# Kernel tuning notes

Hardware: AMD Instinct MI355X
Metric: run time of the kernel (lower is better)

Reference implementation:

```python
import jax, jax.numpy as jnp
import numpy as np

FUTURE_K = 32
NEG_INF = -1e9  # finite large-negative to keep softmax NaN-free on fully-masked rows


def setup_inputs() -> dict:
    key = jax.random.key(0)
    hidden_states = jax.random.normal(key, (4, 2048, 1024), dtype=jnp.float32)
    return {"hidden_states": hidden_states}


def reference(hidden_states) -> jnp.ndarray:
    # Faithful vectorized version of FutureEncoder(summary_method='attention').
    # For each t: window = h[:, t+1 : min(t+1+K, S)], scores = h_t @ window^T,
    # summary_t = softmax(scores) @ window. t = S-1 (empty window) stays zero.
    B, S, D = hidden_states.shape
    offs = jnp.arange(1, FUTURE_K + 1)                 # [K]
    idx = jnp.arange(S)[:, None] + offs[None, :]       # [S, K] future indices t+1..t+K
    valid = idx < S                                     # [S, K]
    idx_c = jnp.minimum(idx, S - 1)
    fw = hidden_states[:, idx_c, :]                     # [B, S, K, D] gathered windows
    scores = jnp.einsum('bsd,bskd->bsk', hidden_states, fw)
    scores = jnp.where(valid[None, :, :], scores, NEG_INF)
    w = jax.nn.softmax(scores, axis=-1)                 # [B, S, K]
    w = jnp.where(valid[None, :, :], w, 0.0)
    out = jnp.einsum('bsk,bskd->bsd', w, fw)            # [B, S, D]
    any_valid = valid.any(axis=-1)                      # [S]; False only at t = S-1
    return jnp.where(any_valid[None, :, None], out, 0.0)
```

## Files before the change

kernel.cpp:

```cpp
#include <hip/hip_runtime.h>
#include <math.h>


constexpr int S_CONST = 2048;
constexpr int D = 1024;
constexpr int G = 16;
constexpr int NTOK = 8192;
constexpr int JW = 48;
constexpr int JP = 49;
constexpr int NW = 8;

typedef short bf16x8 __attribute__((ext_vector_type(8)));
typedef float f32x4  __attribute__((ext_vector_type(4)));
typedef unsigned int u32x4 __attribute__((ext_vector_type(4)));

__device__ inline void cvt8(float4 x0, float4 x1, bf16x8& hi, bf16x8& lo) {
    float xs[8] = {x0.x, x0.y, x0.z, x0.w, x1.x, x1.y, x1.z, x1.w};
    u32x4 hv, lv;
    #pragma unroll
    for (int p = 0; p < 4; ++p) {
        float a = xs[2 * p], b = xs[2 * p + 1];
        unsigned hp;
        asm("v_cvt_pk_bf16_f32 %0, %1, %2" : "=v"(hp) : "v"(a), "v"(b));
        float ha = __builtin_bit_cast(float, hp << 16);
        float hb = __builtin_bit_cast(float, hp & 0xffff0000u);
        float la = a - ha, lb = b - hb;
        unsigned lp;
        asm("v_cvt_pk_bf16_f32 %0, %1, %2" : "=v"(lp) : "v"(la), "v"(lb));
        hv[p] = hp; lv[p] = lp;
    }
    hi = __builtin_bit_cast(bf16x8, hv);
    lo = __builtin_bit_cast(bf16x8, lv);
}

__global__ __launch_bounds__(512, 4)
void future_encoder_kernel(const float* __restrict__ h,
                           float* __restrict__ out) {
    __shared__ float sc[NW * G * JP];
    __shared__ float wm[G * JP];

    int bid = blockIdx.x, nblk = gridDim.x, lb = bid;
    if ((nblk & 7) == 0) {
        int per = nblk >> 3;
        lb = (bid & 7) * per + (bid >> 3);
    }

    const int tid  = threadIdx.x;
    const int w    = tid >> 6;
    const int lane = tid & 63;
    const int t0   = lb * G;
    const int s0   = t0 & (S_CONST - 1);
    const int jlim = (S_CONST - 2) - s0;

    {
        const int d0   = w * 128;
        const int mrow = lane & 15;
        const int q8   = (lane >> 4) * 8;

        const float* A = h + (size_t)(t0 + mrow) * D + d0 + q8;
        int r0 = min(t0 +  1 + mrow, NTOK - 1);
        int r1 = min(t0 + 17 + mrow, NTOK - 1);
        int r2 = min(t0 + 33 + mrow, NTOK - 1);
        const float* B0 = h + (size_t)r0 * D + d0 + q8;
        const float* B1 = h + (size_t)r1 * D + d0 + q8;
        const float* B2 = h + (size_t)r2 * D + d0 + q8;

        f32x4 acc[3] = {{0,0,0,0},{0,0,0,0},{0,0,0,0}};

        float4 xa0 = *(const float4*)(A),      xa1 = *(const float4*)(A + 4);
        float4 x00 = *(const float4*)(B0),     x01 = *(const float4*)(B0 + 4);
        float4 x10 = *(const float4*)(B1),     x11 = *(const float4*)(B1 + 4);
        float4 x20 = *(const float4*)(B2),     x21 = *(const float4*)(B2 + 4);

        #pragma unroll
        for (int kk = 0; kk < 4; ++kk) {
            float4 na0, na1, n00, n01, n10, n11, n20, n21;
            if (kk < 3) {
                const int o = (kk + 1) * 32;
                na0 = *(const float4*)(A  + o); na1 = *(const float4*)(A  + o + 4);
                n00 = *(const float4*)(B0 + o); n01 = *(const float4*)(B0 + o + 4);
                n10 = *(const float4*)(B1 + o); n11 = *(const float4*)(B1 + o + 4);
                n20 = *(const float4*)(B2 + o); n21 = *(const float4*)(B2 + o + 4);
            }

            bf16x8 ah, al;
            cvt8(xa0, xa1, ah, al);

            bf16x8 bh, bl;
            cvt8(x00, x01, bh, bl);
            acc[0] = __builtin_amdgcn_mfma_f32_16x16x32_bf16(ah, bh, acc[0], 0, 0, 0);
            acc[0] = __builtin_amdgcn_mfma_f32_16x16x32_bf16(ah, bl, acc[0], 0, 0, 0);
            acc[0] = __builtin_amdgcn_mfma_f32_16x16x32_bf16(al, bh, acc[0], 0, 0, 0);

            cvt8(x10, x11, bh, bl);
            acc[1] = __builtin_amdgcn_mfma_f32_16x16x32_bf16(ah, bh, acc[1], 0, 0, 0);
            acc[1] = __builtin_amdgcn_mfma_f32_16x16x32_bf16(ah, bl, acc[1], 0, 0, 0);
            acc[1] = __builtin_amdgcn_mfma_f32_16x16x32_bf16(al, bh, acc[1], 0, 0, 0);

            cvt8(x20, x21, bh, bl);
            acc[2] = __builtin_amdgcn_mfma_f32_16x16x32_bf16(ah, bh, acc[2], 0, 0, 0);
            acc[2] = __builtin_amdgcn_mfma_f32_16x16x32_bf16(ah, bl, acc[2], 0, 0, 0);
            acc[2] = __builtin_amdgcn_mfma_f32_16x16x32_bf16(al, bh, acc[2], 0, 0, 0);

            if (kk < 3) {
                xa0 = na0; xa1 = na1;
                x00 = n00; x01 = n01;
                x10 = n10; x11 = n11;
                x20 = n20; x21 = n21;
            }
        }

        #pragma unroll
        for (int t = 0; t < 3; ++t) {
            #pragma unroll
            for (int r = 0; r < 4; ++r) {
                int m = (lane >> 4) * 4 + r;
                int j = t * 16 + (lane & 15);
                sc[(w * G + m) * JP + j] = acc[t][r];
            }
        }
    }
    __syncthreads();

    if (tid < 256) {
        const int i   = tid >> 4;
        const int sub = tid & 15;

        float v[3];
        #pragma unroll
        for (int c = 0; c < 3; ++c) {
            int j = sub + c * 16;
            float s = 0.f;
            #pragma unroll
            for (int ww = 0; ww < NW; ++ww)
                s += sc[(ww * G + i) * JP + j];
            bool valid = (j >= i) && (j <= i + 31) && (j <= jlim);
            v[c] = valid ? s : -1e9f;
        }
        float mx = fmaxf(v[0], fmaxf(v[1], v[2]));
        #pragma unroll
        for (int d = 1; d < 16; d <<= 1) mx = fmaxf(mx, __shfl_xor(mx, d, 16));

        float e[3];
        float sum = 0.f;
        #pragma unroll
        for (int c = 0; c < 3; ++c) { e[c] = __expf(v[c] - mx); sum += e[c]; }
        #pragma unroll
        for (int d = 1; d < 16; d <<= 1) sum += __shfl_xor(sum, d, 16);

        const bool any = (mx > -5e8f);
        const float inv = any ? (1.0f / sum) : 0.f;
        #pragma unroll
        for (int c = 0; c < 3; ++c) {
            int j = sub + c * 16;
            bool valid = (j >= i) && (j <= i + 31) && (j <= jlim);
            wm[i * JP + j] = valid ? e[c] * inv : 0.f;
        }
    }
    __syncthreads();

    {
        const int i0   = (w & 3) * 4;
        const int cc   = (w >> 2) * 2;
        const int doff = cc * 256 + lane * 4;

        float4 a0[2] = {}, a1[2] = {}, a2[2] = {}, a3[2] = {};
        float4 buf[3][2];

        #define LDJ(slot_, jj_) do {                                            \
            int r_ = min(t0 + 1 + i0 + (jj_), NTOK - 1);                        \
            const float* p_ = h + (size_t)r_ * D + doff;                        \
            buf[slot_][0] = *(const float4*)(p_);                               \
            buf[slot_][1] = *(const float4*)(p_ + 256);                         \
        } while (0)

        LDJ(0, 0);
        LDJ(1, 1);

        #pragma unroll
        for (int jj = 0; jj < 35; ++jj) {
            if (jj + 2 < 35) LDJ((jj + 2) % 3, jj + 2);
            const int j = i0 + jj;
            const float w0 = wm[(i0 + 0) * JP + j];
            const float w1 = wm[(i0 + 1) * JP + j];
            const float w2 = wm[(i0 + 2) * JP + j];
            const float w3 = wm[(i0 + 3) * JP + j];
            const float4 fa = buf[jj % 3][0];
            const float4 fb = buf[jj % 3][1];
            a0[0].x += w0 * fa.x; a0[0].y += w0 * fa.y; a0[0].z += w0 * fa.z; a0[0].w += w0 * fa.w;
            a1[0].x += w1 * fa.x; a1[0].y += w1 * fa.y; a1[0].z += w1 * fa.z; a1[0].w += w1 * fa.w;
            a2[0].x += w2 * fa.x; a2[0].y += w2 * fa.y; a2[0].z += w2 * fa.z; a2[0].w += w2 * fa.w;
            a3[0].x += w3 * fa.x; a3[0].y += w3 * fa.y; a3[0].z += w3 * fa.z; a3[0].w += w3 * fa.w;
            a0[1].x += w0 * fb.x; a0[1].y += w0 * fb.y; a0[1].z += w0 * fb.z; a0[1].w += w0 * fb.w;
            a1[1].x += w1 * fb.x; a1[1].y += w1 * fb.y; a1[1].z += w1 * fb.z; a1[1].w += w1 * fb.w;
            a2[1].x += w2 * fb.x; a2[1].y += w2 * fb.y; a2[1].z += w2 * fb.z; a2[1].w += w2 * fb.w;
            a3[1].x += w3 * fb.x; a3[1].y += w3 * fb.y; a3[1].z += w3 * fb.z; a3[1].w += w3 * fb.w;
        }
        #undef LDJ

        float* o0 = out + (size_t)(t0 + i0) * D + doff;
        *(float4*)(o0 + 0 * D)       = a0[0];
        *(float4*)(o0 + 0 * D + 256) = a0[1];
        *(float4*)(o0 + 1 * D)       = a1[0];
        *(float4*)(o0 + 1 * D + 256) = a1[1];
        *(float4*)(o0 + 2 * D)       = a2[0];
        *(float4*)(o0 + 2 * D + 256) = a2[1];
        *(float4*)(o0 + 3 * D)       = a3[0];
        *(float4*)(o0 + 3 * D + 256) = a3[1];
    }
}

extern "C" void kernel_launch(void* const* d_in, const int* in_sizes, int n_in,
                              void* d_out, int out_size, void* d_ws, size_t ws_size,
                              hipStream_t stream) {
    const float* h = (const float*)d_in[0];
    float* out = (float*)d_out;
    const int ntok = in_sizes[0] / D;
    const int blocks = ntok / G;
    future_encoder_kernel<<<blocks, 512, 0, stream>>>(h, out);
}
```

Baseline: 103.9 us.

## Deepen prefetch pipelines and overlap phase-3 loads with softmax

The score GEMM loop now double-buffers two full k-chunks of A/B loads (two chunks in flight instead of one). The weighted-sum phase now has a 7-slot prefetch ring, and its first six row loads are issued before the softmax phase and the barriers, so global memory latency overlaps the reduction and softmax. This costs many more VGPRs (up to 16 extra float4s in phase 1, 14 in phase 3), which may lower occupancy under launch_bounds(512,4) or cause spills.

```diff
diff --git a/kernel.cpp b/kernel.cpp
--- a/kernel.cpp
+++ b/kernel.cpp
@@ -67,48 +67,48 @@
 
         f32x4 acc[3] = {{0,0,0,0},{0,0,0,0},{0,0,0,0}};
 
-        float4 xa0 = *(const float4*)(A),      xa1 = *(const float4*)(A + 4);
-        float4 x00 = *(const float4*)(B0),     x01 = *(const float4*)(B0 + 4);
-        float4 x10 = *(const float4*)(B1),     x11 = *(const float4*)(B1 + 4);
-        float4 x20 = *(const float4*)(B2),     x21 = *(const float4*)(B2 + 4);
+        float4 sA0[8], sA1[8];
+
+        #define ISSUE(slot_, kk_) do {                                          \
+            const int o_ = (kk_) * 32;                                          \
+            slot_[0] = *(const float4*)(A  + o_); slot_[1] = *(const float4*)(A  + o_ + 4); \
+            slot_[2] = *(const float4*)(B0 + o_); slot_[3] = *(const float4*)(B0 + o_ + 4); \
+            slot_[4] = *(const float4*)(B1 + o_); slot_[5] = *(const float4*)(B1 + o_ + 4); \
+            slot_[6] = *(const float4*)(B2 + o_); slot_[7] = *(const float4*)(B2 + o_ + 4); \
+        } while (0)
+
+        ISSUE(sA0, 0);
+        ISSUE(sA1, 1);
 
         #pragma unroll
         for (int kk = 0; kk < 4; ++kk) {
-            float4 na0, na1, n00, n01, n10, n11, n20, n21;
-            if (kk < 3) {
-                const int o = (kk + 1) * 32;
-                na0 = *(const float4*)(A  + o); na1 = *(const float4*)(A  + o + 4);
-                n00 = *(const float4*)(B0 + o); n01 = *(const float4*)(B0 + o + 4);
-                n10 = *(const float4*)(B1 + o); n11 = *(const float4*)(B1 + o + 4);
-                n20 = *(const float4*)(B2 + o); n21 = *(const float4*)(B2 + o + 4);
+            float4* s = (kk & 1) ? sA1 : sA0;
+
+            bf16x8 ah, al, bh, bl;
+            cvt8(s[0], s[1], ah, al);
+            cvt8(s[2], s[3], bh, bl);
+
+            bf16x8 b1h, b1l, b2h, b2l;
+            cvt8(s[4], s[5], b1h, b1l);
+            cvt8(s[6], s[7], b2h, b2l);
+            if (kk < 2) {
+                if (kk & 1) ISSUE(sA1, kk + 2);
+                else        ISSUE(sA0, kk + 2);
             }
 
-            bf16x8 ah, al;
-            cvt8(xa0, xa1, ah, al);
-
-            bf16x8 bh, bl;
-            cvt8(x00, x01, bh, bl);
             acc[0] = __builtin_amdgcn_mfma_f32_16x16x32_bf16(ah, bh, acc[0], 0, 0, 0);
             acc[0] = __builtin_amdgcn_mfma_f32_16x16x32_bf16(ah, bl, acc[0], 0, 0, 0);
             acc[0] = __builtin_amdgcn_mfma_f32_16x16x32_bf16(al, bh, acc[0], 0, 0, 0);
 
-            cvt8(x10, x11, bh, bl);
-            acc[1] = __builtin_amdgcn_mfma_f32_16x16x32_bf16(ah, bh, acc[1], 0, 0, 0);
-            acc[1] = __builtin_amdgcn_mfma_f32_16x16x32_bf16(ah, bl, acc[1], 0, 0, 0);
-            acc[1] = __builtin_amdgcn_mfma_f32_16x16x32_bf16(al, bh, acc[1], 0, 0, 0);
-
-            cvt8(x20, x21, bh, bl);
-            acc[2] = __builtin_amdgcn_mfma_f32_16x16x32_bf16(ah, bh, acc[2], 0, 0, 0);
-            acc[2] = __builtin_amdgcn_mfma_f32_16x16x32_bf16(ah, bl, acc[2], 0, 0, 0);
-            acc[2] = __builtin_amdgcn_mfma_f32_16x16x32_bf16(al, bh, acc[2], 0, 0, 0);
-
-            if (kk < 3) {
-                xa0 = na0; xa1 = na1;
-                x00 = n00; x01 = n01;
-                x10 = n10; x11 = n11;
-                x20 = n20; x21 = n21;
-            }
-        }
+            acc[1] = __builtin_amdgcn_mfma_f32_16x16x32_bf16(ah, b1h, acc[1], 0, 0, 0);
+            acc[1] = __builtin_amdgcn_mfma_f32_16x16x32_bf16(ah, b1l, acc[1], 0, 0, 0);
+            acc[1] = __builtin_amdgcn_mfma_f32_16x16x32_bf16(al, b1h, acc[1], 0, 0, 0);
+
+            acc[2] = __builtin_amdgcn_mfma_f32_16x16x32_bf16(ah, b2h, acc[2], 0, 0, 0);
+            acc[2] = __builtin_amdgcn_mfma_f32_16x16x32_bf16(ah, b2l, acc[2], 0, 0, 0);
+            acc[2] = __builtin_amdgcn_mfma_f32_16x16x32_bf16(al, b2h, acc[2], 0, 0, 0);
+        }
+        #undef ISSUE
 
         #pragma unroll
         for (int t = 0; t < 3; ++t) {
@@ -121,6 +121,21 @@
         }
     }
     __syncthreads();
+
+    const int i0   = (w & 3) * 4;
+    const int cc   = (w >> 2) * 2;
+    const int doff = cc * 256 + lane * 4;
+
+    float4 pbuf[7][2];
+    #define LDJ(slot_, jj_) do {                                                \
+        int r_ = min(t0 + 1 + i0 + (jj_), NTOK - 1);                            \
+        const float* p_ = h + (size_t)r_ * D + doff;                            \
+        pbuf[slot_][0] = *(const float4*)(p_);                                  \
+        pbuf[slot_][1] = *(const float4*)(p_ + 256);                            \
+    } while (0)
+
+    LDJ(0, 0); LDJ(1, 1); LDJ(2, 2); LDJ(3, 3); LDJ(4, 4); LDJ(5, 5);
+    __builtin_amdgcn_sched_barrier(0);
 
     if (tid < 256) {
         const int i   = tid >> 4;
@@ -160,33 +175,18 @@
     __syncthreads();
 
     {
-        const int i0   = (w & 3) * 4;
-        const int cc   = (w >> 2) * 2;
-        const int doff = cc * 256 + lane * 4;
-
         float4 a0[2] = {}, a1[2] = {}, a2[2] = {}, a3[2] = {};
-        float4 buf[3][2];
-
-        #define LDJ(slot_, jj_) do {                                            \
-            int r_ = min(t0 + 1 + i0 + (jj_), NTOK - 1);                        \
-            const float* p_ = h + (size_t)r_ * D + doff;                        \
-            buf[slot_][0] = *(const float4*)(p_);                               \
-            buf[slot_][1] = *(const float4*)(p_ + 256);                         \
-        } while (0)
-
-        LDJ(0, 0);
-        LDJ(1, 1);
 
         #pragma unroll
         for (int jj = 0; jj < 35; ++jj) {
-            if (jj + 2 < 35) LDJ((jj + 2) % 3, jj + 2);
+            if (jj + 6 < 35) LDJ((jj + 6) % 7, jj + 6);
             const int j = i0 + jj;
             const float w0 = wm[(i0 + 0) * JP + j];
             const float w1 = wm[(i0 + 1) * JP + j];
             const float w2 = wm[(i0 + 2) * JP + j];
             const float w3 = wm[(i0 + 3) * JP + j];
-            const float4 fa = buf[jj % 3][0];
-            const float4 fb = buf[jj % 3][1];
+            const float4 fa = pbuf[jj % 7][0];
+            const float4 fb = pbuf[jj % 7][1];
             a0[0].x += w0 * fa.x; a0[0].y += w0 * fa.y; a0[0].z += w0 * fa.z; a0[0].w += w0 * fa.w;
             a1[0].x += w1 * fa.x; a1[0].y += w1 * fa.y; a1[0].z += w1 * fa.z; a1[0].w += w1 * fa.w;
             a2[0].x += w2 * fa.x; a2[0].y += w2 * fa.y; a2[0].z += w2 * fa.z; a2[0].w += w2 * fa.w;
```

Result: no change. 104.5 us (+0.5%).

## Split fused kernel into separate scores/softmax and weighted-sum kernels

Applied to the files above, without the earlier changes.

Breaks the single fused kernel into two launches. The first computes the scores with MFMA using 4 waves, each covering 256 of the D channels, then applies the softmax and writes a compact 32-wide weight row per token to workspace. The second kernel handles 8 tokens per block, with each thread owning 4 channels, and streams the 39 future rows once to accumulate the weighted sums. This aims to improve reuse of the window rows and occupancy in the PV phase. The cost is an extra launch, a round trip of the weights through global memory, and the workspace dependency.

```diff
diff --git a/kernel.cpp b/kernel.cpp
--- a/kernel.cpp
+++ b/kernel.cpp
@@ -6,9 +6,8 @@
 constexpr int D = 1024;
 constexpr int G = 16;
 constexpr int NTOK = 8192;
-constexpr int JW = 48;
 constexpr int JP = 49;
-constexpr int NW = 8;
+constexpr int TB = 8;
 
 typedef short bf16x8 __attribute__((ext_vector_type(8)));
 typedef float f32x4  __attribute__((ext_vector_type(4)));
@@ -33,11 +32,9 @@
     lo = __builtin_bit_cast(bf16x8, lv);
 }
 
-__global__ __launch_bounds__(512, 4)
-void future_encoder_kernel(const float* __restrict__ h,
-                           float* __restrict__ out) {
-    __shared__ float sc[NW * G * JP];
-    __shared__ float wm[G * JP];
+__global__ __launch_bounds__(256, 2)
+void scores_kernel(const float* __restrict__ h, float* __restrict__ wmg) {
+    __shared__ float sc[4 * G * JP];
 
     int bid = blockIdx.x, nblk = gridDim.x, lb = bid;
     if ((nblk & 7) == 0) {
@@ -53,7 +50,7 @@
     const int jlim = (S_CONST - 2) - s0;
 
     {
-        const int d0   = w * 128;
+        const int d0   = w * 256;
         const int mrow = lane & 15;
         const int q8   = (lane >> 4) * 8;
 
@@ -67,15 +64,15 @@
 
         f32x4 acc[3] = {{0,0,0,0},{0,0,0,0},{0,0,0,0}};
 
-        float4 xa0 = *(const float4*)(A),      xa1 = *(const float4*)(A + 4);
-        float4 x00 = *(const float4*)(B0),     x01 = *(const float4*)(B0 + 4);
-        float4 x10 = *(const float4*)(B1),     x11 = *(const float4*)(B1 + 4);
-        float4 x20 = *(const float4*)(B2),     x21 = *(const float4*)(B2 + 4);
-
-        #pragma unroll
-        for (int kk = 0; kk < 4; ++kk) {
+        float4 xa0 = *(const float4*)(A),  xa1 = *(const float4*)(A + 4);
+        float4 x00 = *(const float4*)(B0), x01 = *(const float4*)(B0 + 4);
+        float4 x10 = *(const float4*)(B1), x11 = *(const float4*)(B1 + 4);
+        float4 x20 = *(const float4*)(B2), x21 = *(const float4*)(B2 + 4);
+
+        #pragma unroll
+        for (int kk = 0; kk < 8; ++kk) {
             float4 na0, na1, n00, n01, n10, n11, n20, n21;
-            if (kk < 3) {
+            if (kk < 7) {
                 const int o = (kk + 1) * 32;
                 na0 = *(const float4*)(A  + o); na1 = *(const float4*)(A  + o + 4);
                 n00 = *(const float4*)(B0 + o); n01 = *(const float4*)(B0 + o + 4);
@@ -83,10 +80,9 @@
                 n20 = *(const float4*)(B2 + o); n21 = *(const float4*)(B2 + o + 4);
             }
 
-            bf16x8 ah, al;
+            bf16x8 ah, al, bh, bl;
             cvt8(xa0, xa1, ah, al);
 
-            bf16x8 bh, bl;
             cvt8(x00, x01, bh, bl);
             acc[0] = __builtin_amdgcn_mfma_f32_16x16x32_bf16(ah, bh, acc[0], 0, 0, 0);
             acc[0] = __builtin_amdgcn_mfma_f32_16x16x32_bf16(ah, bl, acc[0], 0, 0, 0);
@@ -102,7 +98,7 @@
             acc[2] = __builtin_amdgcn_mfma_f32_16x16x32_bf16(ah, bl, acc[2], 0, 0, 0);
             acc[2] = __builtin_amdgcn_mfma_f32_16x16x32_bf16(al, bh, acc[2], 0, 0, 0);
 
-            if (kk < 3) {
+            if (kk < 7) {
                 xa0 = na0; xa1 = na1;
                 x00 = n00; x01 = n01;
                 x10 = n10; x11 = n11;
@@ -122,7 +118,7 @@
     }
     __syncthreads();
 
-    if (tid < 256) {
+    {
         const int i   = tid >> 4;
         const int sub = tid & 15;
 
@@ -130,10 +126,8 @@
         #pragma unroll
         for (int c = 0; c < 3; ++c) {
             int j = sub + c * 16;
-            float s = 0.f;
-            #pragma unroll
-            for (int ww = 0; ww < NW; ++ww)
-                s += sc[(ww * G + i) * JP + j];
+            float s = sc[(0 * G + i) * JP + j] + sc[(1 * G + i) * JP + j]
+                    + sc[(2 * G + i) * JP + j] + sc[(3 * G + i) * JP + j];
             bool valid = (j >= i) && (j <= i + 31) && (j <= jlim);
             v[c] = valid ? s : -1e9f;
         }
@@ -150,64 +144,62 @@
 
         const bool any = (mx > -5e8f);
         const float inv = any ? (1.0f / sum) : 0.f;
+
+        float* wrow = wmg + (size_t)(t0 + i) * 32;
         #pragma unroll
         for (int c = 0; c < 3; ++c) {
             int j = sub + c * 16;
-            bool valid = (j >= i) && (j <= i + 31) && (j <= jlim);
-            wm[i * JP + j] = valid ? e[c] * inv : 0.f;
-        }
-    }
+            int k = j - i;
+            if (k >= 0 && k < 32)
+                wrow[k] = (j <= jlim) ? e[c] * inv : 0.f;
+        }
+    }
+}
+
+__global__ __launch_bounds__(256, 4)
+void pv_kernel(const float* __restrict__ h, const float* __restrict__ wm,
+               float* __restrict__ out) {
+    __shared__ float lw[TB * 32];
+
+    int bid = blockIdx.x, nblk = gridDim.x, lb = bid;
+    if ((nblk & 7) == 0) {
+        int per = nblk >> 3;
+        lb = (bid & 7) * per + (bid >> 3);
+    }
+    const int i0   = lb * TB;
+    const int tid  = threadIdx.x;
+    const int doff = tid * 4;
+
+    lw[tid] = wm[(size_t)i0 * 32 + tid];
     __syncthreads();
 
-    {
-        const int i0   = (w & 3) * 4;
-        const int cc   = (w >> 2) * 2;
-        const int doff = cc * 256 + lane * 4;
-
-        float4 a0[2] = {}, a1[2] = {}, a2[2] = {}, a3[2] = {};
-        float4 buf[3][2];
-
-        #define LDJ(slot_, jj_) do {                                            \
-            int r_ = min(t0 + 1 + i0 + (jj_), NTOK - 1);                        \
-            const float* p_ = h + (size_t)r_ * D + doff;                        \
-            buf[slot_][0] = *(const float4*)(p_);                               \
-            buf[slot_][1] = *(const float4*)(p_ + 256);                         \
-        } while (0)
-
-        LDJ(0, 0);
-        LDJ(1, 1);
-
-        #pragma unroll
-        for (int jj = 0; jj < 35; ++jj) {
-            if (jj + 2 < 35) LDJ((jj + 2) % 3, jj + 2);
-            const int j = i0 + jj;
-            const float w0 = wm[(i0 + 0) * JP + j];
-            const float w1 = wm[(i0 + 1) * JP + j];
-            const float w2 = wm[(i0 + 2) * JP + j];
-            const float w3 = wm[(i0 + 3) * JP + j];
-            const float4 fa = buf[jj % 3][0];
-            const float4 fb = buf[jj % 3][1];
-            a0[0].x += w0 * fa.x; a0[0].y += w0 * fa.y; a0[0].z += w0 * fa.z; a0[0].w += w0 * fa.w;
-            a1[0].x += w1 * fa.x; a1[0].y += w1 * fa.y; a1[0].z += w1 * fa.z; a1[0].w += w1 * fa.w;
-            a2[0].x += w2 * fa.x; a2[0].y += w2 * fa.y; a2[0].z += w2 * fa.z; a2[0].w += w2 * fa.w;
-            a3[0].x += w3 * fa.x; a3[0].y += w3 * fa.y; a3[0].z += w3 * fa.z; a3[0].w += w3 * fa.w;
-            a0[1].x += w0 * fb.x; a0[1].y += w0 * fb.y; a0[1].z += w0 * fb.z; a0[1].w += w0 * fb.w;
-            a1[1].x += w1 * fb.x; a1[1].y += w1 * fb.y; a1[1].z += w1 * fb.z; a1[1].w += w1 * fb.w;
-            a2[1].x += w2 * fb.x; a2[1].y += w2 * fb.y; a2[1].z += w2 * fb.z; a2[1].w += w2 * fb.w;
-            a3[1].x += w3 * fb.x; a3[1].y += w3 * fb.y; a3[1].z += w3 * fb.z; a3[1].w += w3 * fb.w;
-        }
-        #undef LDJ
-
-        float* o0 = out + (size_t)(t0 + i0) * D + doff;
-        *(float4*)(o0 + 0 * D)       = a0[0];
-        *(float4*)(o0 + 0 * D + 256) = a0[1];
-        *(float4*)(o0 + 1 * D)       = a1[0];
-        *(float4*)(o0 + 1 * D + 256) = a1[1];
-        *(float4*)(o0 + 2 * D)       = a2[0];
-        *(float4*)(o0 + 2 * D + 256) = a2[1];
-        *(float4*)(o0 + 3 * D)       = a3[0];
-        *(float4*)(o0 + 3 * D + 256) = a3[1];
-    }
+    float4 acc[TB] = {};
+    float4 wv[TB];
+
+    #pragma unroll
+    for (int rr = 0; rr < TB + 31; ++rr) {
+        int r = min(i0 + 1 + rr, NTOK - 1);
+        float4 f = *(const float4*)(h + (size_t)r * D + doff);
+        #pragma unroll
+        for (int t = 0; t < TB; ++t) {
+            const int k = rr - t;
+            if (k >= 0 && k < 32) {
+                if ((k & 3) == 0)
+                    wv[t] = *(const float4*)(&lw[t * 32 + k]);
+                const float wt = ((k & 3) == 0) ? wv[t].x :
+                                 ((k & 3) == 1) ? wv[t].y :
+                                 ((k & 3) == 2) ? wv[t].z : wv[t].w;
+                acc[t].x += wt * f.x;
+                acc[t].y += wt * f.y;
+                acc[t].z += wt * f.z;
+                acc[t].w += wt * f.w;
+            }
+        }
+    }
+
+    #pragma unroll
+    for (int t = 0; t < TB; ++t)
+        *(float4*)(out + (size_t)(i0 + t) * D + doff) = acc[t];
 }
 
 extern "C" void kernel_launch(void* const* d_in, const int* in_sizes, int n_in,
@@ -215,7 +207,9 @@
                               hipStream_t stream) {
     const float* h = (const float*)d_in[0];
     float* out = (float*)d_out;
+    float* wm = (float*)d_ws;
     const int ntok = in_sizes[0] / D;
-    const int blocks = ntok / G;
-    future_encoder_kernel<<<blocks, 512, 0, stream>>>(h, out);
-}
+
+    scores_kernel<<<ntok / G, 256, 0, stream>>>(h, wm);
+    pv_kernel<<<ntok / TB, 256, 0, stream>>>(h, wm, out);
+}
```

New measurement: 104.9 us. About the same (+0.9%).
